# Performance work log

Measured on AMD Instinct MI355X. Metric: run time of the kernel, lower is better.

The kernel has to match this reference:

```python
import jax, jax.numpy as jnp
import numpy as np

N = 8192
STATE_DIM = 64
HIDDENS = [512, 512]
LATENT = 128
TEMP = 1.0
EPS = 1e-12  # torch F.normalize eps


def _linear_params(key, fan_in, fan_out):
    k1, k2 = jax.random.split(key)
    bound = 1.0 / np.sqrt(fan_in)
    W = jax.random.uniform(k1, (fan_in, fan_out), jnp.float32, -bound, bound)
    b = jax.random.uniform(k2, (fan_out,), jnp.float32, -bound, bound)
    return W, b


def setup_inputs() -> dict:
    key = jax.random.key(0)
    ks = jax.random.split(key, 6)
    x = jax.random.normal(ks[0], (N, STATE_DIM), jnp.float32)
    y = jax.random.normal(ks[1], (N, STATE_DIM), jnp.float32)
    # state encoder params (forward uses state_enc for both x and y, as in source)
    W1, b1 = _linear_params(ks[2], STATE_DIM, HIDDENS[0])
    W2, b2 = _linear_params(ks[3], HIDDENS[0], HIDDENS[1])
    W3, b3 = _linear_params(ks[4], HIDDENS[1], LATENT)
    return {"x": x, "y": y, "W1": W1, "b1": b1, "W2": W2, "b2": b2, "W3": W3, "b3": b3}


def _encode(h, W1, b1, W2, b2, W3, b3):
    h = jax.nn.relu(h @ W1 + b1)
    h = jax.nn.relu(h @ W2 + b2)
    return h @ W3 + b3


def _l2norm(z):
    # matches torch F.normalize(dim=-1): z / max(||z||, eps)
    n = jnp.sqrt(jnp.sum(z * z, axis=-1, keepdims=True))
    return z / jnp.maximum(n, EPS)


def reference(x, y, W1, b1, W2, b2, W3, b3):
    zx = _l2norm(_encode(x, W1, b1, W2, b2, W3, b3))  # [N, LATENT]
    zy = _l2norm(_encode(y, W1, b1, W2, b2, W3, b3))  # [N, LATENT]
    # sum(x[:,None,:]*y[None,:,:], -1) == zx @ zy.T, expressed as tiled GEMM
    return jnp.einsum('id,jd->ij', zx, zy) / TEMP  # [N, N]
```

## Files before the change

### kernel.cpp

```cpp
#include <hip/hip_runtime.h>
#include <hip/hip_bf16.h>
#include <cstdint>
#include <cstddef>


typedef unsigned short u16;
typedef __attribute__((ext_vector_type(8))) short bf16x8;
typedef __attribute__((ext_vector_type(4))) float f32x4;

__device__ __forceinline__ u16 f_to_bf16_bits(float f) {
    union { float f; uint32_t u; } v; v.f = f;
    uint32_t lsb = (v.u >> 16) & 1u;
    return (u16)((v.u + 0x7fffu + lsb) >> 16);
}

__global__ __launch_bounds__(256) void cast_f32_bf16_kernel(
    const float* __restrict__ in, u16* __restrict__ out, int n)
{
    int i = blockIdx.x * 256 + threadIdx.x;
    if (i < n) out[i] = f_to_bf16_bits(in[i]);
}

__global__ __launch_bounds__(256) void transpose_cast_kernel(
    const float* __restrict__ in, u16* __restrict__ out, int R, int C)
{
    int idx = blockIdx.x * 256 + threadIdx.x;
    if (idx < R * C) {
        int r = idx / C, c = idx - r * C;
        out[c * R + r] = f_to_bf16_bits(in[r * C + c]);
    }
}

template<bool RELU, bool BIAS, bool OUT_F32>
__global__ __launch_bounds__(256) void gemm_lds_kernel(
    const u16* __restrict__ A, const u16* __restrict__ BT,
    const float* __restrict__ bias,
    u16* __restrict__ Cb, float* __restrict__ Cf,
    int M, int N, int K)
{
    __shared__ u16 lds[16 * 512];
    const int lane = threadIdx.x & 63;
    const int wave = threadIdx.x >> 6;
    const int wm = wave >> 1, wn = wave & 1;
    const int m_base = blockIdx.y * 128;
    const int n_base = blockIdx.x * 128;
    const int mi   = lane & 15;
    const int quad = lane >> 4;

    f32x4 acc[4][4];
    #pragma unroll
    for (int i = 0; i < 4; ++i)
        #pragma unroll
        for (int j = 0; j < 4; ++j)
            acc[i][j] = f32x4{0.f, 0.f, 0.f, 0.f};

    const u16* src[4];
    #pragma unroll
    for (int s = 0; s < 4; ++s) {
        const int t = wave * 4 + s;
        if (t < 8)
            src[s] = A + (size_t)(m_base + t * 16 + mi) * K + quad * 8;
        else
            src[s] = BT + (size_t)(n_base + (t - 8) * 16 + mi) * K + quad * 8;
    }
    u16* dst_base = &lds[wave * 4 * 512];

    for (int k0 = 0; k0 < K; k0 += 32) {
        #pragma unroll
        for (int s = 0; s < 4; ++s) {
            __builtin_amdgcn_global_load_lds(
                (const __attribute__((address_space(1))) void*)(src[s] + k0),
                (__attribute__((address_space(3))) void*)(dst_base + s * 512),
                16, 0, 0);
        }
        __syncthreads();

        bf16x8 af[4], bfr[4];
        #pragma unroll
        for (int i = 0; i < 4; ++i)
            af[i] = *reinterpret_cast<const bf16x8*>(&lds[(wm * 4 + i) * 512 + lane * 8]);
        #pragma unroll
        for (int j = 0; j < 4; ++j)
            bfr[j] = *reinterpret_cast<const bf16x8*>(&lds[(8 + wn * 4 + j) * 512 + lane * 8]);

        #pragma unroll
        for (int i = 0; i < 4; ++i)
            #pragma unroll
            for (int j = 0; j < 4; ++j)
                acc[i][j] = __builtin_amdgcn_mfma_f32_16x16x32_bf16(
                    af[i], bfr[j], acc[i][j], 0, 0, 0);

        __syncthreads();
    }

    const int wm_base = m_base + wm * 64;
    const int wn_base = n_base + wn * 64;
    #pragma unroll
    for (int j = 0; j < 4; ++j) {
        const int col = wn_base + j * 16 + mi;
        float bv = BIAS ? bias[col] : 0.f;
        #pragma unroll
        for (int i = 0; i < 4; ++i) {
            const int row0 = wm_base + i * 16 + quad * 4;
            #pragma unroll
            for (int r = 0; r < 4; ++r) {
                float v = acc[i][j][r] + bv;
                if (RELU) v = fmaxf(v, 0.f);
                if (OUT_F32) Cf[(size_t)(row0 + r) * N + col] = v;
                else         Cb[(size_t)(row0 + r) * N + col] = f_to_bf16_bits(v);
            }
        }
    }
}

__global__ __launch_bounds__(256) void l2norm_kernel(
    const float* __restrict__ z, u16* __restrict__ zn)
{
    const int row  = blockIdx.x * 4 + (threadIdx.x >> 6);
    const int lane = threadIdx.x & 63;
    const float2* zp = reinterpret_cast<const float2*>(z + (size_t)row * 128);
    float2 p = zp[lane];
    float s = p.x * p.x + p.y * p.y;
    #pragma unroll
    for (int off = 32; off > 0; off >>= 1)
        s += __shfl_xor(s, off, 64);
    float inv = 1.0f / fmaxf(sqrtf(s), 1e-12f);
    uint32_t outp = (uint32_t)f_to_bf16_bits(p.x * inv)
                  | ((uint32_t)f_to_bf16_bits(p.y * inv) << 16);
    reinterpret_cast<uint32_t*>(zn + (size_t)row * 128)[lane] = outp;
}

__global__ __launch_bounds__(256) void gemm_nt_k128_kernel(
    const u16* __restrict__ ZX, const u16* __restrict__ ZY,
    float* __restrict__ out)
{
    const int lane = threadIdx.x & 63;
    const int wave = threadIdx.x >> 6;
    const int mi   = lane & 15;
    const int quad = lane >> 4;
    const int wr = wave >> 1, wc = wave & 1;
    const int rb = blockIdx.y * 128 + wr * 64;
    const int cb = blockIdx.x * 128 + wc * 64;

    f32x4 acc[4][4];
    #pragma unroll
    for (int ci = 0; ci < 4; ++ci)
        #pragma unroll
        for (int rj = 0; rj < 4; ++rj)
            acc[ci][rj] = f32x4{0.f, 0.f, 0.f, 0.f};

    const u16* xbase = ZX + (size_t)(rb + mi) * 128 + quad * 8;
    const u16* ybase = ZY + (size_t)(cb + mi) * 128 + quad * 8;

    #pragma unroll
    for (int ks = 0; ks < 4; ++ks) {
        bf16x8 yf[4], xf[4];
        #pragma unroll
        for (int t = 0; t < 4; ++t) {
            yf[t] = *reinterpret_cast<const bf16x8*>(ybase + (size_t)t * 16 * 128 + ks * 32);
            xf[t] = *reinterpret_cast<const bf16x8*>(xbase + (size_t)t * 16 * 128 + ks * 32);
        }
        #pragma unroll
        for (int ci = 0; ci < 4; ++ci)
            #pragma unroll
            for (int rj = 0; rj < 4; ++rj)
                acc[ci][rj] = __builtin_amdgcn_mfma_f32_16x16x32_bf16(
                    yf[ci], xf[rj], acc[ci][rj], 0, 0, 0);
    }

    #pragma unroll
    for (int rj = 0; rj < 4; ++rj) {
        float* orow = out + (size_t)(rb + rj * 16 + mi) * 8192 + cb + quad * 4;
        #pragma unroll
        for (int ci = 0; ci < 4; ++ci)
            *reinterpret_cast<f32x4*>(orow + ci * 16) = acc[ci][rj];
    }
}

extern "C" void kernel_launch(void* const* d_in, const int* in_sizes, int n_in,
                              void* d_out, int out_size, void* d_ws, size_t ws_size,
                              hipStream_t stream)
{
    const float* x  = (const float*)d_in[0];
    const float* y  = (const float*)d_in[1];
    const float* W1 = (const float*)d_in[2];
    const float* b1 = (const float*)d_in[3];
    const float* W2 = (const float*)d_in[4];
    const float* b2 = (const float*)d_in[5];
    const float* W3 = (const float*)d_in[6];
    const float* b3 = (const float*)d_in[7];
    float* out = (float*)d_out;

    u16* ws  = (u16*)d_ws;
    u16* xy  = ws;
    u16* W1T = xy  + (size_t)16384 * 64;
    u16* W2T = W1T + 512 * 64;
    u16* W3T = W2T + 512 * 512;
    u16* h1  = W3T + 128 * 512;
    u16* h2  = h1  + (size_t)16384 * 512;
    u16* zn  = h2  + (size_t)16384 * 512;
    float* z = (float*)(zn + (size_t)16384 * 128);

    dim3 blk(256);

    cast_f32_bf16_kernel<<<(8192 * 64 + 255) / 256, blk, 0, stream>>>(
        x, xy, 8192 * 64);
    cast_f32_bf16_kernel<<<(8192 * 64 + 255) / 256, blk, 0, stream>>>(
        y, xy + (size_t)8192 * 64, 8192 * 64);

    transpose_cast_kernel<<<(64 * 512 + 255) / 256, blk, 0, stream>>>(W1, W1T, 64, 512);
    transpose_cast_kernel<<<(512 * 512 + 255) / 256, blk, 0, stream>>>(W2, W2T, 512, 512);
    transpose_cast_kernel<<<(512 * 128 + 255) / 256, blk, 0, stream>>>(W3, W3T, 512, 128);

    gemm_lds_kernel<true, true, false><<<dim3(4, 128), blk, 0, stream>>>(
        xy, W1T, b1, h1, nullptr, 16384, 512, 64);
    gemm_lds_kernel<true, true, false><<<dim3(4, 128), blk, 0, stream>>>(
        h1, W2T, b2, h2, nullptr, 16384, 512, 512);
    gemm_lds_kernel<false, true, true><<<dim3(1, 128), blk, 0, stream>>>(
        h2, W3T, b3, nullptr, z, 16384, 128, 512);

    l2norm_kernel<<<16384 / 4, blk, 0, stream>>>(z, zn);

    gemm_nt_k128_kernel<<<dim3(64, 64), blk, 0, stream>>>(
        zn, zn + (size_t)8192 * 128, out);
}
```

Measured before the change: 380.8 us.

## Fuse input cast, three-layer MLP encoder and L2 norm into one kernel

Replaces the input cast kernels, the three tiled encoder GEMMs and the separate l2norm pass with a single kernel. In it each wave owns 16 rows, keeps hidden activations in a swizzled per-wave LDS buffer, streams the transposed weights directly from global/L2, and normalizes in registers before writing bf16 latents. This removes the h1/h2/z round trips through HBM and several launches. In exchange it runs only 256 blocks with 64KB LDS each, which means low occupancy. Every wave also rereads the full weight matrices, with little latency hiding in the unroll-1 inner loops.

New measurement: 432.0 us. 1.13x slower.

```diff
diff --git a/kernel.cpp b/kernel.cpp
--- a/kernel.cpp
+++ b/kernel.cpp
@@ -1,5 +1,4 @@
 #include <hip/hip_runtime.h>
-#include <hip/hip_bf16.h>
 #include <cstdint>
 #include <cstddef>
 
@@ -7,6 +6,7 @@
 typedef unsigned short u16;
 typedef __attribute__((ext_vector_type(8))) short bf16x8;
 typedef __attribute__((ext_vector_type(4))) float f32x4;
+typedef __attribute__((ext_vector_type(4))) u16  u16x4;
 
 __device__ __forceinline__ u16 f_to_bf16_bits(float f) {
     union { float f; uint32_t u; } v; v.f = f;
@@ -14,13 +14,6 @@
     return (u16)((v.u + 0x7fffu + lsb) >> 16);
 }
 
-__global__ __launch_bounds__(256) void cast_f32_bf16_kernel(
-    const float* __restrict__ in, u16* __restrict__ out, int n)
-{
-    int i = blockIdx.x * 256 + threadIdx.x;
-    if (i < n) out[i] = f_to_bf16_bits(in[i]);
-}
-
 __global__ __launch_bounds__(256) void transpose_cast_kernel(
     const float* __restrict__ in, u16* __restrict__ out, int R, int C)
 {
@@ -31,103 +24,136 @@
     }
 }
 
-template<bool RELU, bool BIAS, bool OUT_F32>
-__global__ __launch_bounds__(256) void gemm_lds_kernel(
-    const u16* __restrict__ A, const u16* __restrict__ BT,
-    const float* __restrict__ bias,
-    u16* __restrict__ Cb, float* __restrict__ Cf,
-    int M, int N, int K)
-{
-    __shared__ u16 lds[16 * 512];
+__global__ __launch_bounds__(256) void encoder_fused_kernel(
+    const float* __restrict__ X, const float* __restrict__ Y,
+    const u16* __restrict__ W1T, const u16* __restrict__ W2T,
+    const u16* __restrict__ W3T,
+    const float* __restrict__ b1, const float* __restrict__ b2,
+    const float* __restrict__ b3,
+    u16* __restrict__ ZN)
+{
+    __shared__ u16 hbuf[4 * 16 * 512];
     const int lane = threadIdx.x & 63;
     const int wave = threadIdx.x >> 6;
-    const int wm = wave >> 1, wn = wave & 1;
-    const int m_base = blockIdx.y * 128;
-    const int n_base = blockIdx.x * 128;
     const int mi   = lane & 15;
     const int quad = lane >> 4;
-
-    f32x4 acc[4][4];
-    #pragma unroll
-    for (int i = 0; i < 4; ++i)
-        #pragma unroll
-        for (int j = 0; j < 4; ++j)
-            acc[i][j] = f32x4{0.f, 0.f, 0.f, 0.f};
-
-    const u16* src[4];
-    #pragma unroll
-    for (int s = 0; s < 4; ++s) {
-        const int t = wave * 4 + s;
-        if (t < 8)
-            src[s] = A + (size_t)(m_base + t * 16 + mi) * K + quad * 8;
-        else
-            src[s] = BT + (size_t)(n_base + (t - 8) * 16 + mi) * K + quad * 8;
-    }
-    u16* dst_base = &lds[wave * 4 * 512];
-
-    for (int k0 = 0; k0 < K; k0 += 32) {
-        #pragma unroll
-        for (int s = 0; s < 4; ++s) {
-            __builtin_amdgcn_global_load_lds(
-                (const __attribute__((address_space(1))) void*)(src[s] + k0),
-                (__attribute__((address_space(3))) void*)(dst_base + s * 512),
-                16, 0, 0);
-        }
-        __syncthreads();
-
-        bf16x8 af[4], bfr[4];
-        #pragma unroll
-        for (int i = 0; i < 4; ++i)
-            af[i] = *reinterpret_cast<const bf16x8*>(&lds[(wm * 4 + i) * 512 + lane * 8]);
-        #pragma unroll
-        for (int j = 0; j < 4; ++j)
-            bfr[j] = *reinterpret_cast<const bf16x8*>(&lds[(8 + wn * 4 + j) * 512 + lane * 8]);
-
-        #pragma unroll
-        for (int i = 0; i < 4; ++i)
-            #pragma unroll
-            for (int j = 0; j < 4; ++j)
-                acc[i][j] = __builtin_amdgcn_mfma_f32_16x16x32_bf16(
-                    af[i], bfr[j], acc[i][j], 0, 0, 0);
-
-        __syncthreads();
-    }
-
-    const int wm_base = m_base + wm * 64;
-    const int wn_base = n_base + wn * 64;
-    #pragma unroll
-    for (int j = 0; j < 4; ++j) {
-        const int col = wn_base + j * 16 + mi;
-        float bv = BIAS ? bias[col] : 0.f;
-        #pragma unroll
-        for (int i = 0; i < 4; ++i) {
-            const int row0 = wm_base + i * 16 + quad * 4;
-            #pragma unroll
-            for (int r = 0; r < 4; ++r) {
-                float v = acc[i][j][r] + bv;
-                if (RELU) v = fmaxf(v, 0.f);
-                if (OUT_F32) Cf[(size_t)(row0 + r) * N + col] = v;
-                else         Cb[(size_t)(row0 + r) * N + col] = f_to_bf16_bits(v);
+    const int grow = blockIdx.x * 64 + wave * 16 + mi;
+    const float* srow = (grow < 8192) ? (X + (size_t)grow * 64)
+                                      : (Y + (size_t)(grow - 8192) * 64);
+    char* hw = (char*)(hbuf + wave * 16 * 512);
+    const int rbase = mi * 1024;
+    const int swz   = (mi & 7) << 4;
+
+    bf16x8 xf[2];
+    #pragma unroll
+    for (int ks = 0; ks < 2; ++ks) {
+        const float* p = srow + ks * 32 + quad * 8;
+        float4 f0 = *reinterpret_cast<const float4*>(p);
+        float4 f1 = *reinterpret_cast<const float4*>(p + 4);
+        union { u16 u[8]; bf16x8 v; } cv;
+        cv.u[0] = f_to_bf16_bits(f0.x); cv.u[1] = f_to_bf16_bits(f0.y);
+        cv.u[2] = f_to_bf16_bits(f0.z); cv.u[3] = f_to_bf16_bits(f0.w);
+        cv.u[4] = f_to_bf16_bits(f1.x); cv.u[5] = f_to_bf16_bits(f1.y);
+        cv.u[6] = f_to_bf16_bits(f1.z); cv.u[7] = f_to_bf16_bits(f1.w);
+        xf[ks] = cv.v;
+    }
+
+    #pragma unroll 1
+    for (int cbg = 0; cbg < 8; ++cbg) {
+        f32x4 a[4];
+        #pragma unroll
+        for (int j = 0; j < 4; ++j) a[j] = f32x4{0.f, 0.f, 0.f, 0.f};
+        #pragma unroll
+        for (int ks = 0; ks < 2; ++ks) {
+            #pragma unroll
+            for (int j = 0; j < 4; ++j) {
+                const int cb = cbg * 4 + j;
+                bf16x8 wf = *reinterpret_cast<const bf16x8*>(
+                    W1T + (size_t)(cb * 16 + mi) * 64 + ks * 32 + quad * 8);
+                a[j] = __builtin_amdgcn_mfma_f32_16x16x32_bf16(wf, xf[ks], a[j], 0, 0, 0);
             }
         }
-    }
-}
-
-__global__ __launch_bounds__(256) void l2norm_kernel(
-    const float* __restrict__ z, u16* __restrict__ zn)
-{
-    const int row  = blockIdx.x * 4 + (threadIdx.x >> 6);
-    const int lane = threadIdx.x & 63;
-    const float2* zp = reinterpret_cast<const float2*>(z + (size_t)row * 128);
-    float2 p = zp[lane];
-    float s = p.x * p.x + p.y * p.y;
-    #pragma unroll
-    for (int off = 32; off > 0; off >>= 1)
-        s += __shfl_xor(s, off, 64);
-    float inv = 1.0f / fmaxf(sqrtf(s), 1e-12f);
-    uint32_t outp = (uint32_t)f_to_bf16_bits(p.x * inv)
-                  | ((uint32_t)f_to_bf16_bits(p.y * inv) << 16);
-    reinterpret_cast<uint32_t*>(zn + (size_t)row * 128)[lane] = outp;
+        #pragma unroll
+        for (int j = 0; j < 4; ++j) {
+            const int cb = cbg * 4 + j;
+            const float* bp = b1 + cb * 16 + quad * 4;
+            u16x4 pk;
+            #pragma unroll
+            for (int r = 0; r < 4; ++r)
+                pk[r] = f_to_bf16_bits(fmaxf(a[j][r] + bp[r], 0.f));
+            *reinterpret_cast<u16x4*>(hw + rbase + ((cb * 32 + quad * 8) ^ swz)) = pk;
+        }
+    }
+
+    bf16x8 hf[16];
+    #pragma unroll
+    for (int ks = 0; ks < 16; ++ks)
+        hf[ks] = *reinterpret_cast<const bf16x8*>(
+            hw + rbase + ((ks * 64 + quad * 16) ^ swz));
+    #pragma unroll 1
+    for (int cbg = 0; cbg < 8; ++cbg) {
+        f32x4 a[4];
+        #pragma unroll
+        for (int j = 0; j < 4; ++j) a[j] = f32x4{0.f, 0.f, 0.f, 0.f};
+        #pragma unroll 1
+        for (int ks = 0; ks < 16; ++ks) {
+            #pragma unroll
+            for (int j = 0; j < 4; ++j) {
+                const int cb = cbg * 4 + j;
+                bf16x8 wf = *reinterpret_cast<const bf16x8*>(
+                    W2T + (size_t)(cb * 16 + mi) * 512 + ks * 32 + quad * 8);
+                a[j] = __builtin_amdgcn_mfma_f32_16x16x32_bf16(wf, hf[ks], a[j], 0, 0, 0);
+            }
+        }
+        #pragma unroll
+        for (int j = 0; j < 4; ++j) {
+            const int cb = cbg * 4 + j;
+            const float* bp = b2 + cb * 16 + quad * 4;
+            u16x4 pk;
+            #pragma unroll
+            for (int r = 0; r < 4; ++r)
+                pk[r] = f_to_bf16_bits(fmaxf(a[j][r] + bp[r], 0.f));
+            *reinterpret_cast<u16x4*>(hw + rbase + ((cb * 32 + quad * 8) ^ swz)) = pk;
+        }
+    }
+
+    #pragma unroll
+    for (int ks = 0; ks < 16; ++ks)
+        hf[ks] = *reinterpret_cast<const bf16x8*>(
+            hw + rbase + ((ks * 64 + quad * 16) ^ swz));
+    f32x4 zv[8];
+    #pragma unroll
+    for (int cb = 0; cb < 8; ++cb) zv[cb] = f32x4{0.f, 0.f, 0.f, 0.f};
+    #pragma unroll 1
+    for (int ks = 0; ks < 16; ++ks) {
+        #pragma unroll
+        for (int cb = 0; cb < 8; ++cb) {
+            bf16x8 wf = *reinterpret_cast<const bf16x8*>(
+                W3T + (size_t)(cb * 16 + mi) * 512 + ks * 32 + quad * 8);
+            zv[cb] = __builtin_amdgcn_mfma_f32_16x16x32_bf16(wf, hf[ks], zv[cb], 0, 0, 0);
+        }
+    }
+    float s = 0.f;
+    #pragma unroll
+    for (int cb = 0; cb < 8; ++cb) {
+        const float* bp = b3 + cb * 16 + quad * 4;
+        #pragma unroll
+        for (int r = 0; r < 4; ++r) {
+            zv[cb][r] += bp[r];
+            s += zv[cb][r] * zv[cb][r];
+        }
+    }
+    s += __shfl_xor(s, 16, 64);
+    s += __shfl_xor(s, 32, 64);
+    const float inv = 1.0f / fmaxf(sqrtf(s), 1e-12f);
+    u16* zrow = ZN + (size_t)grow * 128;
+    #pragma unroll
+    for (int cb = 0; cb < 8; ++cb) {
+        u16x4 pk;
+        #pragma unroll
+        for (int r = 0; r < 4; ++r) pk[r] = f_to_bf16_bits(zv[cb][r] * inv);
+        *reinterpret_cast<u16x4*>(zrow + cb * 16 + quad * 4) = pk;
+    }
 }
 
 __global__ __launch_bounds__(256) void gemm_nt_k128_kernel(
@@ -192,34 +218,19 @@
     float* out = (float*)d_out;
 
     u16* ws  = (u16*)d_ws;
-    u16* xy  = ws;
-    u16* W1T = xy  + (size_t)16384 * 64;
+    u16* W1T = ws;
     u16* W2T = W1T + 512 * 64;
     u16* W3T = W2T + 512 * 512;
-    u16* h1  = W3T + 128 * 512;
-    u16* h2  = h1  + (size_t)16384 * 512;
-    u16* zn  = h2  + (size_t)16384 * 512;
-    float* z = (float*)(zn + (size_t)16384 * 128);
+    u16* zn  = W3T + 128 * 512;
 
     dim3 blk(256);
 
-    cast_f32_bf16_kernel<<<(8192 * 64 + 255) / 256, blk, 0, stream>>>(
-        x, xy, 8192 * 64);
-    cast_f32_bf16_kernel<<<(8192 * 64 + 255) / 256, blk, 0, stream>>>(
-        y, xy + (size_t)8192 * 64, 8192 * 64);
-
-    transpose_cast_kernel<<<(64 * 512 + 255) / 256, blk, 0, stream>>>(W1, W1T, 64, 512);
-    transpose_cast_kernel<<<(512 * 512 + 255) / 256, blk, 0, stream>>>(W2, W2T, 512, 512);
-    transpose_cast_kernel<<<(512 * 128 + 255) / 256, blk, 0, stream>>>(W3, W3T, 512, 128);
-
-    gemm_lds_kernel<true, true, false><<<dim3(4, 128), blk, 0, stream>>>(
-        xy, W1T, b1, h1, nullptr, 16384, 512, 64);
-    gemm_lds_kernel<true, true, false><<<dim3(4, 128), blk, 0, stream>>>(
-        h1, W2T, b2, h2, nullptr, 16384, 512, 512);
-    gemm_lds_kernel<false, true, true><<<dim3(1, 128), blk, 0, stream>>>(
-        h2, W3T, b3, nullptr, z, 16384, 128, 512);
-
-    l2norm_kernel<<<16384 / 4, blk, 0, stream>>>(z, zn);
+    transpose_cast_kernel<<<128,  blk, 0, stream>>>(W1, W1T, 64, 512);
+    transpose_cast_kernel<<<1024, blk, 0, stream>>>(W2, W2T, 512, 512);
+    transpose_cast_kernel<<<256,  blk, 0, stream>>>(W3, W3T, 512, 128);
+
+    encoder_fused_kernel<<<256, blk, 0, stream>>>(
+        x, y, W1T, W2T, W3T, b1, b2, b3, zn);
 
     gemm_nt_k128_kernel<<<dim3(64, 64), blk, 0, stream>>>(
         zn, zn + (size_t)8192 * 128, out);
```

## Fuse third encoder GEMM with L2 normalization and merge cast/transpose launches

Applied to the files above, without the earlier changes.

Replaces the third layer GEMM plus the separate l2norm kernel with a single kernel in which each wave computes 16 full 128-wide latent rows in registers, adds bias, normalizes, and writes bf16. This removes the fp32 z intermediate round-trip and one launch. The two input casts and three weight transposes are each merged into one launch, cutting launch overhead. The fused kernel launches only 256 blocks and reads W3T straight from global memory without LDS, which may limit occupancy for that stage.

New measurement: 376.9 us. Within noise of the previous version (-1.0%).

```diff
diff --git a/kernel.cpp b/kernel.cpp
--- a/kernel.cpp
+++ b/kernel.cpp
@@ -1,5 +1,4 @@
 #include <hip/hip_runtime.h>
-#include <hip/hip_bf16.h>
 #include <cstdint>
 #include <cstddef>
 
@@ -7,6 +6,7 @@
 typedef unsigned short u16;
 typedef __attribute__((ext_vector_type(8))) short bf16x8;
 typedef __attribute__((ext_vector_type(4))) float f32x4;
+typedef __attribute__((ext_vector_type(4))) u16  u16x4;
 
 __device__ __forceinline__ u16 f_to_bf16_bits(float f) {
     union { float f; uint32_t u; } v; v.f = f;
@@ -14,28 +14,40 @@
     return (u16)((v.u + 0x7fffu + lsb) >> 16);
 }
 
-__global__ __launch_bounds__(256) void cast_f32_bf16_kernel(
-    const float* __restrict__ in, u16* __restrict__ out, int n)
+__global__ __launch_bounds__(256) void cast_inputs_kernel(
+    const float* __restrict__ X, const float* __restrict__ Y,
+    u16* __restrict__ xy)
 {
     int i = blockIdx.x * 256 + threadIdx.x;
-    if (i < n) out[i] = f_to_bf16_bits(in[i]);
-}
-
-__global__ __launch_bounds__(256) void transpose_cast_kernel(
-    const float* __restrict__ in, u16* __restrict__ out, int R, int C)
+    float v = (i < 524288) ? X[i] : Y[i - 524288];
+    xy[i] = f_to_bf16_bits(v);
+}
+
+__global__ __launch_bounds__(256) void transpose_weights_kernel(
+    const float* __restrict__ W1, const float* __restrict__ W2,
+    const float* __restrict__ W3,
+    u16* __restrict__ W1T, u16* __restrict__ W2T, u16* __restrict__ W3T)
 {
     int idx = blockIdx.x * 256 + threadIdx.x;
-    if (idx < R * C) {
-        int r = idx / C, c = idx - r * C;
-        out[c * R + r] = f_to_bf16_bits(in[r * C + c]);
-    }
-}
-
-template<bool RELU, bool BIAS, bool OUT_F32>
+    if (idx < 32768) {
+        int r = idx >> 9, c = idx & 511;
+        W1T[c * 64 + r] = f_to_bf16_bits(W1[idx]);
+    } else if (idx < 294912) {
+        int k = idx - 32768;
+        int r = k >> 9, c = k & 511;
+        W2T[c * 512 + r] = f_to_bf16_bits(W2[k]);
+    } else if (idx < 360448) {
+        int k = idx - 294912;
+        int r = k >> 7, c = k & 127;
+        W3T[c * 512 + r] = f_to_bf16_bits(W3[k]);
+    }
+}
+
+template<bool RELU>
 __global__ __launch_bounds__(256) void gemm_lds_kernel(
     const u16* __restrict__ A, const u16* __restrict__ BT,
     const float* __restrict__ bias,
-    u16* __restrict__ Cb, float* __restrict__ Cf,
+    u16* __restrict__ Cb,
     int M, int N, int K)
 {
     __shared__ u16 lds[16 * 512];
@@ -98,7 +110,7 @@
     #pragma unroll
     for (int j = 0; j < 4; ++j) {
         const int col = wn_base + j * 16 + mi;
-        float bv = BIAS ? bias[col] : 0.f;
+        float bv = bias[col];
         #pragma unroll
         for (int i = 0; i < 4; ++i) {
             const int row0 = wm_base + i * 16 + quad * 4;
@@ -106,28 +118,65 @@
             for (int r = 0; r < 4; ++r) {
                 float v = acc[i][j][r] + bv;
                 if (RELU) v = fmaxf(v, 0.f);
-                if (OUT_F32) Cf[(size_t)(row0 + r) * N + col] = v;
-                else         Cb[(size_t)(row0 + r) * N + col] = f_to_bf16_bits(v);
+                Cb[(size_t)(row0 + r) * N + col] = f_to_bf16_bits(v);
             }
         }
     }
 }
 
-__global__ __launch_bounds__(256) void l2norm_kernel(
-    const float* __restrict__ z, u16* __restrict__ zn)
-{
-    const int row  = blockIdx.x * 4 + (threadIdx.x >> 6);
+__global__ __launch_bounds__(256) void gemm3_l2norm_kernel(
+    const u16* __restrict__ H2, const u16* __restrict__ W3T,
+    const float* __restrict__ b3, u16* __restrict__ ZN)
+{
     const int lane = threadIdx.x & 63;
-    const float2* zp = reinterpret_cast<const float2*>(z + (size_t)row * 128);
-    float2 p = zp[lane];
-    float s = p.x * p.x + p.y * p.y;
-    #pragma unroll
-    for (int off = 32; off > 0; off >>= 1)
-        s += __shfl_xor(s, off, 64);
-    float inv = 1.0f / fmaxf(sqrtf(s), 1e-12f);
-    uint32_t outp = (uint32_t)f_to_bf16_bits(p.x * inv)
-                  | ((uint32_t)f_to_bf16_bits(p.y * inv) << 16);
-    reinterpret_cast<uint32_t*>(zn + (size_t)row * 128)[lane] = outp;
+    const int wave = threadIdx.x >> 6;
+    const int mi   = lane & 15;
+    const int quad = lane >> 4;
+    const int grow = blockIdx.x * 64 + wave * 16 + mi;
+
+    bf16x8 hf[16];
+    const u16* hbase = H2 + (size_t)grow * 512 + quad * 8;
+    #pragma unroll
+    for (int ks = 0; ks < 16; ++ks)
+        hf[ks] = *reinterpret_cast<const bf16x8*>(hbase + ks * 32);
+
+    f32x4 zv[8];
+    #pragma unroll
+    for (int cb = 0; cb < 8; ++cb) zv[cb] = f32x4{0.f, 0.f, 0.f, 0.f};
+
+    const u16* wbase = W3T + (size_t)mi * 512 + quad * 8;
+    #pragma unroll 1
+    for (int ks = 0; ks < 16; ++ks) {
+        #pragma unroll
+        for (int cb = 0; cb < 8; ++cb) {
+            bf16x8 wf = *reinterpret_cast<const bf16x8*>(
+                wbase + (size_t)cb * 16 * 512 + ks * 32);
+            zv[cb] = __builtin_amdgcn_mfma_f32_16x16x32_bf16(wf, hf[ks], zv[cb], 0, 0, 0);
+        }
+    }
+
+    float s = 0.f;
+    #pragma unroll
+    for (int cb = 0; cb < 8; ++cb) {
+        const float* bp = b3 + cb * 16 + quad * 4;
+        #pragma unroll
+        for (int r = 0; r < 4; ++r) {
+            zv[cb][r] += bp[r];
+            s += zv[cb][r] * zv[cb][r];
+        }
+    }
+    s += __shfl_xor(s, 16, 64);
+    s += __shfl_xor(s, 32, 64);
+    const float inv = 1.0f / fmaxf(sqrtf(s), 1e-12f);
+
+    u16* zrow = ZN + (size_t)grow * 128;
+    #pragma unroll
+    for (int cb = 0; cb < 8; ++cb) {
+        u16x4 pk;
+        #pragma unroll
+        for (int r = 0; r < 4; ++r) pk[r] = f_to_bf16_bits(zv[cb][r] * inv);
+        *reinterpret_cast<u16x4*>(zrow + cb * 16 + quad * 4) = pk;
+    }
 }
 
 __global__ __launch_bounds__(256) void gemm_nt_k128_kernel(
@@ -199,27 +248,20 @@
     u16* h1  = W3T + 128 * 512;
     u16* h2  = h1  + (size_t)16384 * 512;
     u16* zn  = h2  + (size_t)16384 * 512;
-    float* z = (float*)(zn + (size_t)16384 * 128);
 
     dim3 blk(256);
 
-    cast_f32_bf16_kernel<<<(8192 * 64 + 255) / 256, blk, 0, stream>>>(
-        x, xy, 8192 * 64);
-    cast_f32_bf16_kernel<<<(8192 * 64 + 255) / 256, blk, 0, stream>>>(
-        y, xy + (size_t)8192 * 64, 8192 * 64);
-
-    transpose_cast_kernel<<<(64 * 512 + 255) / 256, blk, 0, stream>>>(W1, W1T, 64, 512);
-    transpose_cast_kernel<<<(512 * 512 + 255) / 256, blk, 0, stream>>>(W2, W2T, 512, 512);
-    transpose_cast_kernel<<<(512 * 128 + 255) / 256, blk, 0, stream>>>(W3, W3T, 512, 128);
-
-    gemm_lds_kernel<true, true, false><<<dim3(4, 128), blk, 0, stream>>>(
-        xy, W1T, b1, h1, nullptr, 16384, 512, 64);
-    gemm_lds_kernel<true, true, false><<<dim3(4, 128), blk, 0, stream>>>(
-        h1, W2T, b2, h2, nullptr, 16384, 512, 512);
-    gemm_lds_kernel<false, true, true><<<dim3(1, 128), blk, 0, stream>>>(
-        h2, W3T, b3, nullptr, z, 16384, 128, 512);
-
-    l2norm_kernel<<<16384 / 4, blk, 0, stream>>>(z, zn);
+    cast_inputs_kernel<<<4096, blk, 0, stream>>>(x, y, xy);
+
+    transpose_weights_kernel<<<1408, blk, 0, stream>>>(
+        W1, W2, W3, W1T, W2T, W3T);
+
+    gemm_lds_kernel<true><<<dim3(4, 128), blk, 0, stream>>>(
+        xy, W1T, b1, h1, 16384, 512, 64);
+    gemm_lds_kernel<true><<<dim3(4, 128), blk, 0, stream>>>(
+        h1, W2T, b2, h2, 16384, 512, 512);
+
+    gemm3_l2norm_kernel<<<256, blk, 0, stream>>>(h2, W3T, b3, zn);
 
     gemm_nt_k128_kernel<<<dim3(64, 64), blk, 0, stream>>>(
         zn, zn + (size_t)8192 * 128, out);
```
